# Optimization experiments

Measured on AMD Instinct MI355X. Metric: run time of the kernel, lower is better.

## Reference

```python
import jax, jax.numpy as jnp
import numpy as np

ALPHA = 0.2
GAMMA = 1.5
EPS = 1e-8
NORM = jnp.array([0.1, 0.1, 0.2, 0.2], dtype=jnp.float32)


def calc_iou(a, b):
    # a: [A,4] anchors, b: [M,4] gt boxes -> [A,M] IoU
    area_b = (b[:, 2] - b[:, 0]) * (b[:, 3] - b[:, 1])          # [M]
    area_a = (a[:, 2] - a[:, 0]) * (a[:, 3] - a[:, 1])          # [A]
    iw = jnp.clip(jnp.minimum(a[:, 2:3], b[None, :, 2]) - jnp.maximum(a[:, 0:1], b[None, :, 0]), 0.0)
    ih = jnp.clip(jnp.minimum(a[:, 3:4], b[None, :, 3]) - jnp.maximum(a[:, 1:2], b[None, :, 1]), 0.0)
    inter = iw * ih
    ua = jnp.clip(area_a[:, None] + area_b[None, :] - inter, EPS)
    return inter / ua


def setup_inputs() -> dict:
    key = jax.random.key(0)
    k1, k2, k3, k4, k5, k6, k7, k8 = jax.random.split(key, 8)
    B, A, C, M = 8, 120000, 20, 32
    # anchors: plausible boxes on a ~1000px image
    acx = jax.random.uniform(k1, (A,), minval=0.0, maxval=1000.0)
    acy = jax.random.uniform(k2, (A,), minval=0.0, maxval=1000.0)
    awh = jax.random.uniform(k3, (A, 2), minval=16.0, maxval=256.0)
    anchors = jnp.stack([acx - awh[:, 0] / 2, acy - awh[:, 1] / 2,
                         acx + awh[:, 0] / 2, acy + awh[:, 1] / 2], axis=1)[None]  # [1,A,4]
    # annotations: [B,M,5], last col = label, some padded with -1
    gxy = jax.random.uniform(k4, (B, M, 2), minval=0.0, maxval=900.0)
    gwh = jax.random.uniform(k5, (B, M, 2), minval=20.0, maxval=120.0)
    lbl = jax.random.randint(k6, (B, M), 0, C).astype(jnp.float32)
    lbl = jnp.where(jnp.arange(M)[None, :] >= 28, -1.0, lbl)  # 4 padded GT per image
    annotations = jnp.concatenate([gxy, gxy + gwh, lbl[..., None]], axis=-1)
    classifications = jax.random.uniform(k7, (B, A, C), minval=0.01, maxval=0.99)
    regressions = jax.random.normal(k8, (B, A, 4), dtype=jnp.float32)
    return {"classifications": classifications, "regressions": regressions,
            "anchors": anchors, "annotations": annotations}


def reference(classifications, regressions, anchors, annotations):
    anc = anchors[0]                                  # [A,4]
    aw = anc[:, 2] - anc[:, 0]
    ah = anc[:, 3] - anc[:, 1]
    acx = anc[:, 0] + 0.5 * aw
    acy = anc[:, 1] + 0.5 * ah
    C = classifications.shape[-1]
    cls_ids = jnp.arange(C)

    def per_image(cls, reg, ann):
        valid = ann[:, 4] != -1.0                     # [M]
        num_valid = valid.sum()
        clsc = jnp.clip(cls, EPS, 1.0 - EPS)          # [A,C]
        iou = calc_iou(anc, ann[:, :4])               # [A,M]
        iou = jnp.where(valid[None, :], iou, -1.0)    # never match padded GT
        iou_max = iou.max(axis=1)                     # [A]
        iou_arg = iou.argmax(axis=1)                  # [A]
        pos = iou_max >= 0.5
        num_pos = pos.sum()

        assigned = ann[iou_arg]                       # [A,5]
        lbl = assigned[:, 4].astype(jnp.int32)
        # targets: -1 ignore, 0 negative, one-hot 1 for positives
        tgt = jnp.where((iou_max < 0.4)[:, None], 0.0, -1.0)
        tgt = jnp.where(pos[:, None], 0.0, tgt)
        tgt = jnp.where(pos[:, None] & (cls_ids[None, :] == lbl[:, None]), 1.0, tgt)

        af = jnp.where(tgt == 1.0, ALPHA, 1.0 - ALPHA)
        fw = af * jnp.where(tgt == 1.0, 1.0 - clsc, clsc) ** GAMMA
        bce = -(tgt * jnp.log(clsc) + (1.0 - tgt) * jnp.log(1.0 - clsc))
        cls_loss = jnp.where(tgt != -1.0, fw * bce, 0.0).sum()
        cls_loss = cls_loss / jnp.clip(num_pos.astype(clsc.dtype), 1.0)

        gw_raw = assigned[:, 2] - assigned[:, 0]
        gh_raw = assigned[:, 3] - assigned[:, 1]
        gcx = assigned[:, 0] + 0.5 * gw_raw
        gcy = assigned[:, 1] + 0.5 * gh_raw
        gw = jnp.clip(gw_raw, 1.0)
        gh = jnp.clip(gh_raw, 1.0)
        rt = jnp.stack([(gcx - acx) / aw, (gcy - acy) / ah,
                        jnp.log(gw / aw), jnp.log(gh / ah)], axis=1) / NORM  # [A,4]
        diff = jnp.abs(rt - reg)
        sl1 = jnp.where(diff <= 1.0 / 9.0, 0.5 * 9.0 * diff * diff, diff - 0.5 / 9.0)
        reg_sum = jnp.where(pos[:, None], sl1, 0.0).sum()
        reg_loss = reg_sum / jnp.clip(4.0 * num_pos.astype(clsc.dtype), 1.0)
        reg_loss = jnp.where(num_pos > 0, reg_loss, 0.0)

        cls_loss = jnp.where(num_valid > 0, cls_loss, 0.0)
        reg_loss = jnp.where(num_valid > 0, reg_loss, 0.0)
        return cls_loss, reg_loss

    cl, rl = jax.vmap(per_image)(classifications, regressions, annotations)
    return cl.mean(keepdims=True), rl.mean(keepdims=True)
```

## Files before the change

kernel.cpp:

```cpp
#include <hip/hip_runtime.h>
#include <math.h>

constexpr int C = 20;
constexpr int M = 32;
#define LN2F 0.69314718055994530942f

__global__ __launch_bounds__(256) void focal_main(
    const float* __restrict__ cls,
    const float* __restrict__ reg,
    const float* __restrict__ anc,
    const float* __restrict__ ann,
    float* __restrict__ part,
    int A)
{
    __shared__ float4 s_gbox[M];
    __shared__ float  s_garea[M];
    __shared__ int    s_glbl[M];
    __shared__ float  s_red[4 * 3];

    const int b   = blockIdx.y;
    const int tid = threadIdx.x;

    if (tid < M) {
        const float* ap = ann + (size_t)b * M * 5 + (size_t)tid * 5;
        float x1 = ap[0], y1 = ap[1], x2 = ap[2], y2 = ap[3];
        const float lb = ap[4];
        s_glbl[tid] = (int)lb;
        if (lb == -1.0f) { x1 = 0.f; y1 = 0.f; x2 = 0.f; y2 = 0.f; }
        s_gbox[tid]  = make_float4(x1, y1, x2, y2);
        s_garea[tid] = (x2 - x1) * (y2 - y1);
    }
    __syncthreads();

    const int a = blockIdx.x * 256 + tid;

    float clsSum = 0.f, regSum = 0.f, posf = 0.f;

    if (a < A) {
        const float4 av = *(const float4*)(anc + (size_t)a * 4);
        const float aw  = av.z - av.x;
        const float ah  = av.w - av.y;
        const float acx = av.x + 0.5f * aw;
        const float acy = av.y + 0.5f * ah;
        const float area_a = aw * ah;

        float n_b = -1.0f, d_b = 1.0f;
        int   bi = 0;
        #pragma unroll 8
        for (int j = 0; j < M; ++j) {
            const float4 g  = s_gbox[j];
            const float  ab = s_garea[j];
            const float iw = fmaxf(fminf(av.z, g.z) - fmaxf(av.x, g.x), 0.f);
            const float ih = fmaxf(fminf(av.w, g.w) - fmaxf(av.y, g.y), 0.f);
            const float inter = iw * ih;
            const float ua = fmaxf(area_a + ab - inter, 1e-8f);
            if (inter * d_b > n_b * ua) { n_b = inter; d_b = ua; bi = j; }
        }
        const float bv = n_b * __frcp_rn(d_b);
        const bool pos    = bv >= 0.5f;
        const bool ignore = (bv >= 0.4f) && !pos;
        const int  lbl    = s_glbl[bi];

        if (!ignore) {
            const float* cp = cls + ((size_t)b * A + a) * C;
            float sum = 0.f;
            float p_t = 0.5f;
            #pragma unroll
            for (int k = 0; k < C / 4; ++k) {
                const float4 v = *(const float4*)(cp + k * 4);
                const float pv4[4] = {v.x, v.y, v.z, v.w};
                #pragma unroll
                for (int u = 0; u < 4; ++u) {
                    const int c = k * 4 + u;
                    const float p = fminf(fmaxf(pv4[u], 1e-8f), 1.0f - 1e-8f);
                    sum += p * __builtin_amdgcn_sqrtf(p) * (-__log2f(1.0f - p));
                    p_t = (c == lbl) ? p : p_t;
                }
            }
            sum *= 0.8f;
            if (pos) {
                const float q = 1.0f - p_t;
                sum -= 0.8f * p_t * __builtin_amdgcn_sqrtf(p_t) * (-__log2f(q));
                sum += 0.2f * q   * __builtin_amdgcn_sqrtf(q)   * (-__log2f(p_t));
            }
            clsSum = sum * LN2F;
        }

        if (pos) {
            posf = 1.0f;
            const float4 g = s_gbox[bi];
            const float gwr = g.z - g.x, ghr = g.w - g.y;
            const float gcx = g.x + 0.5f * gwr, gcy = g.y + 0.5f * ghr;
            const float gw = fmaxf(gwr, 1.f), gh = fmaxf(ghr, 1.f);
            float rt[4];
            rt[0] = ((gcx - acx) / aw) / 0.1f;
            rt[1] = ((gcy - acy) / ah) / 0.1f;
            rt[2] = __logf(gw / aw) / 0.2f;
            rt[3] = __logf(gh / ah) / 0.2f;
            const float4 rv = *(const float4*)(reg + ((size_t)b * A + a) * 4);
            const float rr[4] = {rv.x, rv.y, rv.z, rv.w};
            #pragma unroll
            for (int u = 0; u < 4; ++u) {
                const float d = fabsf(rt[u] - rr[u]);
                regSum += (d <= (float)(1.0 / 9.0)) ? (4.5f * d * d)
                                                    : (d - (float)(0.5 / 9.0));
            }
        }
    }

    #pragma unroll
    for (int off = 32; off > 0; off >>= 1) {
        clsSum += __shfl_down(clsSum, off, 64);
        regSum += __shfl_down(regSum, off, 64);
        posf   += __shfl_down(posf,   off, 64);
    }
    const int wave = tid >> 6;
    const int lane = tid & 63;
    if (lane == 0) {
        s_red[wave*3+0] = clsSum;
        s_red[wave*3+1] = regSum;
        s_red[wave*3+2] = posf;
    }
    __syncthreads();
    if (tid == 0) {
        float cs = 0.f, rs = 0.f, ps = 0.f;
        #pragma unroll
        for (int w2 = 0; w2 < 4; ++w2) {
            cs += s_red[w2*3+0];
            rs += s_red[w2*3+1];
            ps += s_red[w2*3+2];
        }
        const size_t slot = ((size_t)b * gridDim.x + blockIdx.x) * 4;
        *(float4*)(part + slot) = make_float4(cs, rs, ps, 0.f);
    }
}

__global__ __launch_bounds__(1024) void focal_final(
    const float* __restrict__ part,
    const float* __restrict__ ann,
    float* __restrict__ out, int B, int nblk)
{
    __shared__ float s_sum[8][2][3];
    __shared__ float s_f[256];
    __shared__ float s_c[8], s_r[8];

    const int tid = threadIdx.x;
    const int g   = tid >> 7;
    const int i   = tid & 127;

    float cs = 0.f, rs = 0.f, ps = 0.f;
    if (g < B) {
        for (int bx = i; bx < nblk; bx += 128) {
            const float4 v = *(const float4*)(part + ((size_t)g * nblk + bx) * 4);
            cs += v.x; rs += v.y; ps += v.z;
        }
    }
    #pragma unroll
    for (int off = 32; off > 0; off >>= 1) {
        cs += __shfl_down(cs, off, 64);
        rs += __shfl_down(rs, off, 64);
        ps += __shfl_down(ps, off, 64);
    }
    const int lane = tid & 63;
    const int wv   = (tid >> 6) & 1;
    if (lane == 0 && g < 8) {
        s_sum[g][wv][0] = cs; s_sum[g][wv][1] = rs; s_sum[g][wv][2] = ps;
    }

    if (tid < 256) {
        float f = 0.f;
        if (tid < B * M) {
            const int bb = tid >> 5, j = tid & 31;
            f = (ann[(size_t)bb * M * 5 + (size_t)j * 5 + 4] != -1.0f) ? 1.f : 0.f;
        }
        s_f[tid] = f;
    }
    __syncthreads();

    if (tid < B) {
        const float S  = s_sum[tid][0][0] + s_sum[tid][1][0];
        const float R  = s_sum[tid][0][1] + s_sum[tid][1][1];
        const float np = s_sum[tid][0][2] + s_sum[tid][1][2];
        float nv = 0.f;
        #pragma unroll
        for (int j = 0; j < M; ++j) nv += s_f[tid * M + j];
        float cl = S / fmaxf(np, 1.f);
        float rl = (np > 0.f) ? R / fmaxf(4.f * np, 1.f) : 0.f;
        if (nv == 0.f) { cl = 0.f; rl = 0.f; }
        s_c[tid] = cl; s_r[tid] = rl;
    }
    __syncthreads();

    if (tid == 0) {
        float ca = 0.f, ra = 0.f;
        for (int b2 = 0; b2 < B; ++b2) { ca += s_c[b2]; ra += s_r[b2]; }
        out[0] = ca / (float)B;
        out[1] = ra / (float)B;
    }
}

extern "C" void kernel_launch(void* const* d_in, const int* in_sizes, int n_in,
                              void* d_out, int out_size, void* d_ws, size_t ws_size,
                              hipStream_t stream) {
    const float* cls = (const float*)d_in[0];
    const float* reg = (const float*)d_in[1];
    const float* anc = (const float*)d_in[2];
    const float* ann = (const float*)d_in[3];
    const int A = in_sizes[2] / 4;
    const int B = in_sizes[3] / (M * 5);
    const int nblk = (A + 255) / 256;

    float* part = (float*)d_ws;

    dim3 grid(nblk, B);
    focal_main<<<grid, dim3(256), 0, stream>>>(cls, reg, anc, ann, part, A);
    focal_final<<<1, dim3(1024), 0, stream>>>(part, ann, (float*)d_out, B, nblk);
}
```

Measured before the change: 128.1 us.

## Process two anchors per thread, compact valid GTs, broadcast boxes via readlane

Each thread now handles two anchors, and each block covers twice as many anchors. Valid ground-truth boxes are compacted with a ballot so the IoU loop stops at the valid count. Box coordinates are broadcast from registers with readlane instead of being read from LDS, and classification loads are issued before the IoU loop so their latency overlaps the compute. The label probability is re-read from memory only for positive anchors, which removes the per-class select. The cost is higher register pressure and half as many blocks.

```diff
diff --git a/kernel.cpp b/kernel.cpp
--- a/kernel.cpp
+++ b/kernel.cpp
@@ -3,7 +3,74 @@
 
 constexpr int C = 20;
 constexpr int M = 32;
+constexpr int KPA  = 2;
+constexpr int BLKA = 256 * KPA;
 #define LN2F 0.69314718055994530942f
+
+__device__ __forceinline__ float rl(float v, int j) {
+    return __int_as_float(__builtin_amdgcn_readlane(__float_as_int(v), j));
+}
+
+__device__ __forceinline__ void anchor_tail(
+    bool ok, float4 av, float n_b, float d_b, int bi,
+    const float* __restrict__ cp, const float* __restrict__ regp,
+    const float4* cv,
+    const float4* s_gbox, const int* s_glbl,
+    float& clsSum, float& regSum, float& posf)
+{
+    if (!ok) return;
+    const float bv     = n_b * __frcp_rn(d_b);
+    const bool  pos    = bv >= 0.5f;
+    const bool  ignore = (bv >= 0.4f) && !pos;
+
+    if (!ignore) {
+        float sum = 0.f;
+        #pragma unroll
+        for (int k = 0; k < C / 4; ++k) {
+            const float4 v4 = cv[k];
+            const float pv4[4] = {v4.x, v4.y, v4.z, v4.w};
+            #pragma unroll
+            for (int u = 0; u < 4; ++u) {
+                const float p = fminf(fmaxf(pv4[u], 1e-8f), 1.0f - 1e-8f);
+                sum += p * __builtin_amdgcn_sqrtf(p) * (-__log2f(1.0f - p));
+            }
+        }
+        sum *= 0.8f;
+        if (pos) {
+            const int   lbl = s_glbl[bi];
+            const float p_t = fminf(fmaxf(cp[lbl], 1e-8f), 1.0f - 1e-8f);
+            const float q   = 1.0f - p_t;
+            sum -= 0.8f * p_t * __builtin_amdgcn_sqrtf(p_t) * (-__log2f(q));
+            sum += 0.2f * q   * __builtin_amdgcn_sqrtf(q)   * (-__log2f(p_t));
+        }
+        clsSum += sum * LN2F;
+    }
+
+    if (pos) {
+        posf += 1.0f;
+        const float aw  = av.z - av.x;
+        const float ah  = av.w - av.y;
+        const float acx = av.x + 0.5f * aw;
+        const float acy = av.y + 0.5f * ah;
+        const float4 g = s_gbox[bi];
+        const float gwr = g.z - g.x, ghr = g.w - g.y;
+        const float gcx = g.x + 0.5f * gwr, gcy = g.y + 0.5f * ghr;
+        const float gw = fmaxf(gwr, 1.f), gh = fmaxf(ghr, 1.f);
+        float rt[4];
+        rt[0] = ((gcx - acx) / aw) / 0.1f;
+        rt[1] = ((gcy - acy) / ah) / 0.1f;
+        rt[2] = __logf(gw / aw) / 0.2f;
+        rt[3] = __logf(gh / ah) / 0.2f;
+        const float4 rv = *(const float4*)regp;
+        const float rr[4] = {rv.x, rv.y, rv.z, rv.w};
+        #pragma unroll
+        for (int u = 0; u < 4; ++u) {
+            const float d = fabsf(rt[u] - rr[u]);
+            regSum += (d <= (float)(1.0 / 9.0)) ? (4.5f * d * d)
+                                                : (d - (float)(0.5 / 9.0));
+        }
+    }
+}
 
 __global__ __launch_bounds__(256) void focal_main(
     const float* __restrict__ cls,
@@ -14,99 +81,92 @@
     int A)
 {
     __shared__ float4 s_gbox[M];
-    __shared__ float  s_garea[M];
     __shared__ int    s_glbl[M];
+    __shared__ int    s_cnt;
     __shared__ float  s_red[4 * 3];
 
     const int b   = blockIdx.y;
     const int tid = threadIdx.x;
 
-    if (tid < M) {
-        const float* ap = ann + (size_t)b * M * 5 + (size_t)tid * 5;
-        float x1 = ap[0], y1 = ap[1], x2 = ap[2], y2 = ap[3];
-        const float lb = ap[4];
-        s_glbl[tid] = (int)lb;
-        if (lb == -1.0f) { x1 = 0.f; y1 = 0.f; x2 = 0.f; y2 = 0.f; }
-        s_gbox[tid]  = make_float4(x1, y1, x2, y2);
-        s_garea[tid] = (x2 - x1) * (y2 - y1);
-    }
-    __syncthreads();
-
-    const int a = blockIdx.x * 256 + tid;
+    if (tid < 64) {
+        bool  v  = false;
+        float x1 = 0.f, y1 = 0.f, x2 = 0.f, y2 = 0.f, lb = -1.f;
+        if (tid < M) {
+            const float* ap = ann + (size_t)b * M * 5 + (size_t)tid * 5;
+            x1 = ap[0]; y1 = ap[1]; x2 = ap[2]; y2 = ap[3]; lb = ap[4];
+            v = (lb != -1.0f);
+            s_gbox[tid] = make_float4(0.f, 0.f, 0.f, 0.f);
+            s_glbl[tid] = 0;
+        }
+        const unsigned long long mask = __ballot(v);
+        if (v) {
+            const int pos = __popcll(mask & ((1ull << tid) - 1ull));
+            s_gbox[pos] = make_float4(x1, y1, x2, y2);
+            s_glbl[pos] = (int)lb;
+        }
+        if (tid == 0) s_cnt = (int)__popcll(mask);
+    }
+    __syncthreads();
+
+    const float4 gb    = s_gbox[tid & 31];
+    const float  garea = (gb.z - gb.x) * (gb.w - gb.y);
+    const int    cnt   = __builtin_amdgcn_readfirstlane(s_cnt);
+
+    const int a0 = blockIdx.x * BLKA + tid;
+    const int a1 = a0 + 256;
+    const bool ok0 = a0 < A;
+    const bool ok1 = a1 < A;
+
+    float4 av0 = make_float4(0.f, 0.f, 0.f, 0.f);
+    float4 av1 = av0;
+    if (ok0) av0 = *(const float4*)(anc + (size_t)a0 * 4);
+    if (ok1) av1 = *(const float4*)(anc + (size_t)a1 * 4);
+    const float area0 = (av0.z - av0.x) * (av0.w - av0.y);
+    const float area1 = (av1.z - av1.x) * (av1.w - av1.y);
+
+    const float* cp0 = cls + ((size_t)b * A + a0) * C;
+    const float* cp1 = cls + ((size_t)b * A + a1) * C;
+    float4 cv0[C / 4], cv1[C / 4];
+    if (ok0) {
+        #pragma unroll
+        for (int k = 0; k < C / 4; ++k) cv0[k] = ((const float4*)cp0)[k];
+    }
+    if (ok1) {
+        #pragma unroll
+        for (int k = 0; k < C / 4; ++k) cv1[k] = ((const float4*)cp1)[k];
+    }
+
+    float n0 = -1.0f, d0 = 1.0f, n1 = -1.0f, d1 = 1.0f;
+    int   bi0 = 0, bi1 = 0;
+    #pragma unroll
+    for (int j = 0; j < M; ++j) {
+        if (j >= cnt) break;
+        const float gx1 = rl(gb.x, j);
+        const float gy1 = rl(gb.y, j);
+        const float gx2 = rl(gb.z, j);
+        const float gy2 = rl(gb.w, j);
+        const float gab = rl(garea, j);
+        {
+            const float iw = fmaxf(fminf(av0.z, gx2) - fmaxf(av0.x, gx1), 0.f);
+            const float ih = fmaxf(fminf(av0.w, gy2) - fmaxf(av0.y, gy1), 0.f);
+            const float inter = iw * ih;
+            const float ua = fmaxf(area0 + gab - inter, 1e-8f);
+            if (inter * d0 > n0 * ua) { n0 = inter; d0 = ua; bi0 = j; }
+        }
+        {
+            const float iw = fmaxf(fminf(av1.z, gx2) - fmaxf(av1.x, gx1), 0.f);
+            const float ih = fmaxf(fminf(av1.w, gy2) - fmaxf(av1.y, gy1), 0.f);
+            const float inter = iw * ih;
+            const float ua = fmaxf(area1 + gab - inter, 1e-8f);
+            if (inter * d1 > n1 * ua) { n1 = inter; d1 = ua; bi1 = j; }
+        }
+    }
 
     float clsSum = 0.f, regSum = 0.f, posf = 0.f;
-
-    if (a < A) {
-        const float4 av = *(const float4*)(anc + (size_t)a * 4);
-        const float aw  = av.z - av.x;
-        const float ah  = av.w - av.y;
-        const float acx = av.x + 0.5f * aw;
-        const float acy = av.y + 0.5f * ah;
-        const float area_a = aw * ah;
-
-        float n_b = -1.0f, d_b = 1.0f;
-        int   bi = 0;
-        #pragma unroll 8
-        for (int j = 0; j < M; ++j) {
-            const float4 g  = s_gbox[j];
-            const float  ab = s_garea[j];
-            const float iw = fmaxf(fminf(av.z, g.z) - fmaxf(av.x, g.x), 0.f);
-            const float ih = fmaxf(fminf(av.w, g.w) - fmaxf(av.y, g.y), 0.f);
-            const float inter = iw * ih;
-            const float ua = fmaxf(area_a + ab - inter, 1e-8f);
-            if (inter * d_b > n_b * ua) { n_b = inter; d_b = ua; bi = j; }
-        }
-        const float bv = n_b * __frcp_rn(d_b);
-        const bool pos    = bv >= 0.5f;
-        const bool ignore = (bv >= 0.4f) && !pos;
-        const int  lbl    = s_glbl[bi];
-
-        if (!ignore) {
-            const float* cp = cls + ((size_t)b * A + a) * C;
-            float sum = 0.f;
-            float p_t = 0.5f;
-            #pragma unroll
-            for (int k = 0; k < C / 4; ++k) {
-                const float4 v = *(const float4*)(cp + k * 4);
-                const float pv4[4] = {v.x, v.y, v.z, v.w};
-                #pragma unroll
-                for (int u = 0; u < 4; ++u) {
-                    const int c = k * 4 + u;
-                    const float p = fminf(fmaxf(pv4[u], 1e-8f), 1.0f - 1e-8f);
-                    sum += p * __builtin_amdgcn_sqrtf(p) * (-__log2f(1.0f - p));
-                    p_t = (c == lbl) ? p : p_t;
-                }
-            }
-            sum *= 0.8f;
-            if (pos) {
-                const float q = 1.0f - p_t;
-                sum -= 0.8f * p_t * __builtin_amdgcn_sqrtf(p_t) * (-__log2f(q));
-                sum += 0.2f * q   * __builtin_amdgcn_sqrtf(q)   * (-__log2f(p_t));
-            }
-            clsSum = sum * LN2F;
-        }
-
-        if (pos) {
-            posf = 1.0f;
-            const float4 g = s_gbox[bi];
-            const float gwr = g.z - g.x, ghr = g.w - g.y;
-            const float gcx = g.x + 0.5f * gwr, gcy = g.y + 0.5f * ghr;
-            const float gw = fmaxf(gwr, 1.f), gh = fmaxf(ghr, 1.f);
-            float rt[4];
-            rt[0] = ((gcx - acx) / aw) / 0.1f;
-            rt[1] = ((gcy - acy) / ah) / 0.1f;
-            rt[2] = __logf(gw / aw) / 0.2f;
-            rt[3] = __logf(gh / ah) / 0.2f;
-            const float4 rv = *(const float4*)(reg + ((size_t)b * A + a) * 4);
-            const float rr[4] = {rv.x, rv.y, rv.z, rv.w};
-            #pragma unroll
-            for (int u = 0; u < 4; ++u) {
-                const float d = fabsf(rt[u] - rr[u]);
-                regSum += (d <= (float)(1.0 / 9.0)) ? (4.5f * d * d)
-                                                    : (d - (float)(0.5 / 9.0));
-            }
-        }
-    }
+    anchor_tail(ok0, av0, n0, d0, bi0, cp0, reg + ((size_t)b * A + a0) * 4,
+                cv0, s_gbox, s_glbl, clsSum, regSum, posf);
+    anchor_tail(ok1, av1, n1, d1, bi1, cp1, reg + ((size_t)b * A + a1) * 4,
+                cv1, s_gbox, s_glbl, clsSum, regSum, posf);
 
     #pragma unroll
     for (int off = 32; off > 0; off >>= 1) {
@@ -185,9 +245,9 @@
         #pragma unroll
         for (int j = 0; j < M; ++j) nv += s_f[tid * M + j];
         float cl = S / fmaxf(np, 1.f);
-        float rl = (np > 0.f) ? R / fmaxf(4.f * np, 1.f) : 0.f;
-        if (nv == 0.f) { cl = 0.f; rl = 0.f; }
-        s_c[tid] = cl; s_r[tid] = rl;
+        float rl2 = (np > 0.f) ? R / fmaxf(4.f * np, 1.f) : 0.f;
+        if (nv == 0.f) { cl = 0.f; rl2 = 0.f; }
+        s_c[tid] = cl; s_r[tid] = rl2;
     }
     __syncthreads();
 
@@ -208,7 +268,7 @@
     const float* ann = (const float*)d_in[3];
     const int A = in_sizes[2] / 4;
     const int B = in_sizes[3] / (M * 5);
-    const int nblk = (A + 255) / 256;
+    const int nblk = (A + BLKA - 1) / BLKA;
 
     float* part = (float*)d_ws;
 
```

After: 134.2 us. 1.05x slower.

## Compact valid GT boxes, broadcast via readlane, prefetch class scores early

Applied to the files above, without the earlier changes.

Uses a wave ballot to pack the valid ground-truth boxes in front and loops only over that count, which skips the padded boxes. Box coordinates and areas are held in registers and broadcast with readlane instead of read from LDS each iteration. The class-score loads are issued before the IoU loop so their memory latency overlaps the compute, and p_t is fetched once with an indexed load only for positive anchors instead of a per-class select. The trade-off is higher register pressure from holding 20 prefetched floats, and a variable trip count where the loop was fully static.

```diff
diff --git a/kernel.cpp b/kernel.cpp
--- a/kernel.cpp
+++ b/kernel.cpp
@@ -4,6 +4,10 @@
 constexpr int C = 20;
 constexpr int M = 32;
 #define LN2F 0.69314718055994530942f
+
+__device__ __forceinline__ float rl(float v, int j) {
+    return __int_as_float(__builtin_amdgcn_readlane(__float_as_int(v), j));
+}
 
 __global__ __launch_bounds__(256) void focal_main(
     const float* __restrict__ cls,
@@ -14,23 +18,36 @@
     int A)
 {
     __shared__ float4 s_gbox[M];
-    __shared__ float  s_garea[M];
     __shared__ int    s_glbl[M];
+    __shared__ int    s_cnt;
     __shared__ float  s_red[4 * 3];
 
     const int b   = blockIdx.y;
     const int tid = threadIdx.x;
 
-    if (tid < M) {
-        const float* ap = ann + (size_t)b * M * 5 + (size_t)tid * 5;
-        float x1 = ap[0], y1 = ap[1], x2 = ap[2], y2 = ap[3];
-        const float lb = ap[4];
-        s_glbl[tid] = (int)lb;
-        if (lb == -1.0f) { x1 = 0.f; y1 = 0.f; x2 = 0.f; y2 = 0.f; }
-        s_gbox[tid]  = make_float4(x1, y1, x2, y2);
-        s_garea[tid] = (x2 - x1) * (y2 - y1);
-    }
-    __syncthreads();
+    if (tid < 64) {
+        bool  v  = false;
+        float x1 = 0.f, y1 = 0.f, x2 = 0.f, y2 = 0.f, lb = -1.f;
+        if (tid < M) {
+            const float* ap = ann + (size_t)b * M * 5 + (size_t)tid * 5;
+            x1 = ap[0]; y1 = ap[1]; x2 = ap[2]; y2 = ap[3]; lb = ap[4];
+            v = (lb != -1.0f);
+            s_gbox[tid] = make_float4(0.f, 0.f, 0.f, 0.f);
+            s_glbl[tid] = 0;
+        }
+        const unsigned long long mask = __ballot(v);
+        if (v) {
+            const int pos = __popcll(mask & ((1ull << tid) - 1ull));
+            s_gbox[pos] = make_float4(x1, y1, x2, y2);
+            s_glbl[pos] = (int)lb;
+        }
+        if (tid == 0) s_cnt = (int)__popcll(mask);
+    }
+    __syncthreads();
+
+    const float4 gb    = s_gbox[tid & 31];
+    const float  garea = (gb.z - gb.x) * (gb.w - gb.y);
+    const int    cnt   = __builtin_amdgcn_readfirstlane(s_cnt);
 
     const int a = blockIdx.x * 256 + tid;
 
@@ -40,46 +57,49 @@
         const float4 av = *(const float4*)(anc + (size_t)a * 4);
         const float aw  = av.z - av.x;
         const float ah  = av.w - av.y;
-        const float acx = av.x + 0.5f * aw;
-        const float acy = av.y + 0.5f * ah;
         const float area_a = aw * ah;
+
+        const float* cp = cls + ((size_t)b * A + a) * C;
+        float4 cv[C / 4];
+        #pragma unroll
+        for (int k = 0; k < C / 4; ++k) cv[k] = ((const float4*)cp)[k];
 
         float n_b = -1.0f, d_b = 1.0f;
         int   bi = 0;
-        #pragma unroll 8
-        for (int j = 0; j < M; ++j) {
-            const float4 g  = s_gbox[j];
-            const float  ab = s_garea[j];
-            const float iw = fmaxf(fminf(av.z, g.z) - fmaxf(av.x, g.x), 0.f);
-            const float ih = fmaxf(fminf(av.w, g.w) - fmaxf(av.y, g.y), 0.f);
+        #pragma unroll 4
+        for (int j = 0; j < cnt; ++j) {
+            const float gx1 = rl(gb.x, j);
+            const float gy1 = rl(gb.y, j);
+            const float gx2 = rl(gb.z, j);
+            const float gy2 = rl(gb.w, j);
+            const float gab = rl(garea, j);
+            const float iw = fmaxf(fminf(av.z, gx2) - fmaxf(av.x, gx1), 0.f);
+            const float ih = fmaxf(fminf(av.w, gy2) - fmaxf(av.y, gy1), 0.f);
             const float inter = iw * ih;
-            const float ua = fmaxf(area_a + ab - inter, 1e-8f);
+            const float ua = fmaxf(area_a + gab - inter, 1e-8f);
             if (inter * d_b > n_b * ua) { n_b = inter; d_b = ua; bi = j; }
         }
         const float bv = n_b * __frcp_rn(d_b);
         const bool pos    = bv >= 0.5f;
         const bool ignore = (bv >= 0.4f) && !pos;
-        const int  lbl    = s_glbl[bi];
 
         if (!ignore) {
-            const float* cp = cls + ((size_t)b * A + a) * C;
             float sum = 0.f;
-            float p_t = 0.5f;
             #pragma unroll
             for (int k = 0; k < C / 4; ++k) {
-                const float4 v = *(const float4*)(cp + k * 4);
-                const float pv4[4] = {v.x, v.y, v.z, v.w};
+                const float4 v4 = cv[k];
+                const float pv4[4] = {v4.x, v4.y, v4.z, v4.w};
                 #pragma unroll
                 for (int u = 0; u < 4; ++u) {
-                    const int c = k * 4 + u;
                     const float p = fminf(fmaxf(pv4[u], 1e-8f), 1.0f - 1e-8f);
                     sum += p * __builtin_amdgcn_sqrtf(p) * (-__log2f(1.0f - p));
-                    p_t = (c == lbl) ? p : p_t;
                 }
             }
             sum *= 0.8f;
             if (pos) {
-                const float q = 1.0f - p_t;
+                const int   lbl = s_glbl[bi];
+                const float p_t = fminf(fmaxf(cp[lbl], 1e-8f), 1.0f - 1e-8f);
+                const float q   = 1.0f - p_t;
                 sum -= 0.8f * p_t * __builtin_amdgcn_sqrtf(p_t) * (-__log2f(q));
                 sum += 0.2f * q   * __builtin_amdgcn_sqrtf(q)   * (-__log2f(p_t));
             }
@@ -88,6 +108,8 @@
 
         if (pos) {
             posf = 1.0f;
+            const float acx = av.x + 0.5f * aw;
+            const float acy = av.y + 0.5f * ah;
             const float4 g = s_gbox[bi];
             const float gwr = g.z - g.x, ghr = g.w - g.y;
             const float gcx = g.x + 0.5f * gwr, gcy = g.y + 0.5f * ghr;
@@ -184,10 +206,10 @@
         float nv = 0.f;
         #pragma unroll
         for (int j = 0; j < M; ++j) nv += s_f[tid * M + j];
-        float cl = S / fmaxf(np, 1.f);
-        float rl = (np > 0.f) ? R / fmaxf(4.f * np, 1.f) : 0.f;
-        if (nv == 0.f) { cl = 0.f; rl = 0.f; }
-        s_c[tid] = cl; s_r[tid] = rl;
+        float cl  = S / fmaxf(np, 1.f);
+        float rl2 = (np > 0.f) ? R / fmaxf(4.f * np, 1.f) : 0.f;
+        if (nv == 0.f) { cl = 0.f; rl2 = 0.f; }
+        s_c[tid] = cl; s_r[tid] = rl2;
     }
     __syncthreads();
 
```

Measured after the change: 135.6 us. +5.9%, slower.
